# Kernel tuning notes

Hardware: AMD Instinct MI355X
Metric: run time of the kernel (lower is better)

The kernel has to match this reference:

```python
import jax, jax.numpy as jnp
import numpy as np

E = 256  # embedding_dim

def setup_inputs() -> dict:
    key = jax.random.key(0)
    k1, k2, k3 = jax.random.split(key, 3)
    B, P, N, D = 32, 4, 1024, E
    x = jax.random.normal(k1, (B, P, N, D), dtype=jnp.float32)
    W_qkv = jax.random.normal(k2, (D, 1 + 2 * E), dtype=jnp.float32) * (1.0 / np.sqrt(D))
    b_qkv = jnp.zeros((1 + 2 * E,), dtype=jnp.float32)
    W_o = jax.random.normal(k3, (E, E), dtype=jnp.float32) * (1.0 / np.sqrt(E))
    b_o = jnp.zeros((E,), dtype=jnp.float32)
    return {"x": x, "W_qkv": W_qkv, "b_qkv": b_qkv, "W_o": W_o, "b_o": b_o}

def reference(x, W_qkv, b_qkv, W_o, b_o):
    # qkv projection: [B,P,N,D] @ [D,1+2E] -> [B,P,N,1+2E]
    qkv = jnp.einsum('bpnd,de->bpne', x, W_qkv) + b_qkv
    q = qkv[..., :1]                 # [B,P,N,1]
    k = qkv[..., 1:1 + E]            # [B,P,N,E]
    v = jax.nn.relu(qkv[..., 1 + E:])  # [B,P,N,E]
    # softmax over patch axis N (axis=2)
    context_scores = jax.nn.softmax(q, axis=2)
    # context vector: sum over N of k * scores -> [B,P,1,E]
    context_vector = jnp.sum(k * context_scores, axis=2, keepdims=True)
    # broadcast-multiply with relu(v): [B,P,N,E] * [B,P,1,E]
    updated_values = v * context_vector
    # output projection
    out = jnp.einsum('bpnd,de->bpne', updated_values, W_o) + b_o
    return out
```

## Files before the change

### kernel.cpp

```cpp
#include <hip/hip_runtime.h>
#include <hip/hip_bf16.h>

typedef float f32x4 __attribute__((ext_vector_type(4)));
typedef short s16x8 __attribute__((ext_vector_type(8)));
typedef __bf16 bf16x8 __attribute__((ext_vector_type(8)));
typedef unsigned short u16;

#define NSEQ 1024
#define EDIM 256

#define WAITVM(N) asm volatile("s_waitcnt vmcnt(" #N ")" ::: "memory")

__device__ __forceinline__ u16 f2bf(float f){
  union { float f; unsigned u; } v; v.f = f;
  unsigned r = v.u + 0x7FFF + ((v.u >> 16) & 1);
  return (u16)(r >> 16);
}
__device__ __forceinline__ float bf2f(u16 b){
  union { float f; unsigned u; } v; v.u = ((unsigned)b) << 16;
  return v.f;
}

template <typename V>
__device__ __forceinline__ auto mfma_impl(V a, V b, f32x4 c, int)
    -> decltype(__builtin_amdgcn_mfma_f32_16x16x32_bf16(a, b, c, 0, 0, 0)) {
  return __builtin_amdgcn_mfma_f32_16x16x32_bf16(a, b, c, 0, 0, 0);
}
template <typename V>
__device__ __forceinline__ f32x4 mfma_impl(V a, V b, f32x4 c, long){
  bf16x8 ab = __builtin_bit_cast(bf16x8, a);
  bf16x8 bb = __builtin_bit_cast(bf16x8, b);
  return __builtin_amdgcn_mfma_f32_16x16x32_bf16(ab, bb, c, 0, 0, 0);
}
__device__ __forceinline__ f32x4 mfma16(s16x8 a, s16x8 b, f32x4 c){
  return mfma_impl(a, b, c, 0);
}

__device__ __forceinline__ void gload_lds16(const u16* g, u16* l){
  __builtin_amdgcn_global_load_lds((const __attribute__((address_space(1))) void*)g,
                                   (__attribute__((address_space(3))) void*)l, 16, 0, 0);
}

__global__ void k0_prep(const float* __restrict__ Wqkv, const float* __restrict__ Wo,
                        u16* __restrict__ wvf, u16* __restrict__ wof, float* __restrict__ wqc){
  int t = blockIdx.x * 256 + threadIdx.x;
  if (t < 16384){
    int which = t >> 13;
    int slot  = t & 8191;
    int l  = slot & 63;
    int nt = (slot >> 6) & 1;
    int ks = (slot >> 7) & 7;
    int c  = (slot >> 10) & 7;
    int row = ks*32 + 8*(l>>4);
    int col = c*32 + nt*16 + (l&15);
    s16x8 o8;
    if (which == 0){
      for (int j=0;j<8;j++) o8[j] = (short)f2bf(Wqkv[(size_t)(row+j)*513 + 257 + col]);
      *(s16x8*)(wvf + (size_t)slot*8) = o8;
    } else {
      for (int j=0;j<8;j++) o8[j] = (short)f2bf(Wo[(size_t)(row+j)*256 + col]);
      *(s16x8*)(wof + (size_t)slot*8) = o8;
    }
  } else if (t < 16384 + 256){
    int d = t - 16384;
    wqc[d] = Wqkv[(size_t)d*513];
  }
}

__global__ void k1_qfrag(const float* __restrict__ x, const float* __restrict__ wqc,
                         const float* __restrict__ bqkv, u16* __restrict__ xf, float* __restrict__ q){
  int bp = blockIdx.x >> 6, rt = blockIdx.x & 63;
  const float* xt = x + ((size_t)bp*NSEQ + rt*16) * EDIM;
  __shared__ float xl[16][260];
  int tid = threadIdx.x;
  for (int i=0;i<4;i++){
    int idx = tid + i*256;
    float4 vv = ((const float4*)xt)[idx];
    int row = idx >> 6, c4 = idx & 63;
    *(float4*)&xl[row][c4*4] = vv;
  }
  __syncthreads();
  int l = tid & 63, w = tid >> 6;
  int lo = l & 15, hi = l >> 4;
  for (int kk=0;kk<2;kk++){
    int ks = w*2 + kk;
    int k0 = ks*32 + 8*hi;
    s16x8 o8;
    for (int j=0;j<8;j++) o8[j] = (short)f2bf(xl[lo][k0+j]);
    size_t fo = ((((size_t)bp*64 + rt)*8 + ks)*64 + l) * 8;
    *(s16x8*)(xf + fo) = o8;
  }
  int c = l*4;
  float4 wv4 = *(const float4*)(wqc + c);
  float b0 = bqkv[0];
  for (int r=0;r<4;r++){
    int row = w*4 + r;
    float4 xv = *(float4*)&xl[row][c];
    float p = xv.x*wv4.x + xv.y*wv4.y + xv.z*wv4.z + xv.w*wv4.w;
    for (int o=32;o;o>>=1) p += __shfl_down(p, o);
    if (l == 0) q[(size_t)bp*NSEQ + rt*16 + row] = p + b0;
  }
}

__global__ __launch_bounds__(512) void k234(
    const u16* __restrict__ xf, const float* __restrict__ q,
    const float* __restrict__ Wqkv, const float* __restrict__ bqkv,
    float* __restrict__ cv){
  int bp = blockIdx.x;
  int tid = threadIdx.x, l = tid & 63, w = tid >> 6;
  int lo = l & 15, hi = l >> 4;
  __shared__ float sm[1024];
  __shared__ float red[16];
  __shared__ float tl[256];
  __shared__ float cvp[2][256];

  float2 v = ((const float2*)(q + (size_t)bp*NSEQ))[tid];
  float m = fmaxf(v.x, v.y);
  for (int o=32;o;o>>=1) m = fmaxf(m, __shfl_xor(m, o));
  if (l == 0) red[w] = m;
  __syncthreads();
  m = red[0];
#pragma unroll
  for (int i=1;i<8;i++) m = fmaxf(m, red[i]);
  float e0 = expf(v.x - m), e1 = expf(v.y - m);
  float ss = e0 + e1;
  for (int o=32;o;o>>=1) ss += __shfl_xor(ss, o);
  if (l == 0) red[8 + w] = ss;
  __syncthreads();
  float tot = red[8];
#pragma unroll
  for (int i=1;i<8;i++) tot += red[8 + i];
  float inv = 1.0f / tot;
  sm[2*tid]   = e0 * inv;
  sm[2*tid+1] = e1 * inv;
  __syncthreads();

  float acc[8];
#pragma unroll
  for (int j=0;j<8;j++) acc[j] = 0.f;
  const u16* base = xf + (((size_t)bp*64)*8 + w)*512 + (size_t)l*8;
  for (int rt=0; rt<64; rt++){
    s16x8 d8 = *(const s16x8*)(base + (size_t)rt*4096);
    float sv = sm[rt*16 + lo];
#pragma unroll
    for (int j=0;j<8;j++) acc[j] += sv * bf2f((u16)d8[j]);
  }
#pragma unroll
  for (int j=0;j<8;j++)
    for (int mm=1;mm<16;mm<<=1) acc[j] += __shfl_xor(acc[j], mm);
  if (lo == 0){
#pragma unroll
    for (int j=0;j<8;j++) tl[w*32 + 8*hi + j] = acc[j];
  }
  __syncthreads();

  int e = tid & 255, half = tid >> 8;
  float a = 0.f;
  for (int d = half*128; d < half*128 + 128; d++)
    a += tl[d] * Wqkv[(size_t)d*513 + 1 + e];
  cvp[half][e] = a;
  __syncthreads();
  if (tid < 256)
    cv[(size_t)bp*EDIM + tid] = bqkv[1 + tid] + cvp[0][tid] + cvp[1][tid];
}

__global__ __launch_bounds__(256, 2) void k5_main(
    const u16* __restrict__ xf, const u16* __restrict__ wvf, const u16* __restrict__ wof,
    const float* __restrict__ bqkv, const float* __restrict__ bo,
    const float* __restrict__ cv, float* __restrict__ out){
  int bp = blockIdx.x >> 3, rt = blockIdx.x & 7;
  int tid = threadIdx.x, l = tid & 63, w = tid >> 6;
  int lo = l & 15, hi = l >> 4;
  __shared__ u16 WBUF[3][16][512];
  __shared__ u16 HB[4][2][16][40];

  s16x8 af0[8], af1[8];
  {
    const u16* src0 = xf + ((((size_t)bp*64 + rt*8 + 2*w + 0)*8)*64 + l)*8;
    const u16* src1 = src0 + 4096;
#pragma unroll
    for (int ks=0;ks<8;ks++){
      af0[ks] = *(const s16x8*)(src0 + (size_t)ks*512);
      af1[ks] = *(const s16x8*)(src1 + (size_t)ks*512);
    }
  }
  const float* cvb = cv + (size_t)bp*EDIM;
  float* ob0 = out + ((size_t)bp*NSEQ + (rt*8 + 2*w + 0)*16) * EDIM;
  float* ob1 = ob0 + 16*EDIM;

  auto stage = [&](int chunk, int buf){
    const u16* base = (chunk < 8) ? (wvf + (size_t)chunk*8192) : (wof + (size_t)(chunk-8)*8192);
    const u16* gsrc = base + (size_t)(w*4)*512 + l*8;
#pragma unroll
    for (int i=0;i<4;i++) gload_lds16(gsrc + i*512, &WBUF[buf][w*4 + i][0]);
  };

  stage(0, 0);
  stage(1, 1);
  WAITVM(4);
  __builtin_amdgcn_s_barrier();
  __builtin_amdgcn_sched_barrier(0);

  s16x8 hf0[8], hf1[8];

#pragma unroll
  for (int c=0;c<16;c++){
    const int buf = c % 3;
    f32x4 acc00 = {0.f,0.f,0.f,0.f}, acc01 = acc00, acc10 = acc00, acc11 = acc00;
    auto do_mfma = [&](const s16x8 (&A0)[8], const s16x8 (&A1)[8]){
      __builtin_amdgcn_s_setprio(1);
#pragma unroll
      for (int ks=0;ks<8;ks++){
        s16x8 b0 = *(const s16x8*)&WBUF[buf][ks*2 + 0][l*8];
        s16x8 b1 = *(const s16x8*)&WBUF[buf][ks*2 + 1][l*8];
        acc00 = mfma16(A0[ks], b0, acc00);
        acc10 = mfma16(A1[ks], b0, acc10);
        acc01 = mfma16(A0[ks], b1, acc01);
        acc11 = mfma16(A1[ks], b1, acc11);
      }
      __builtin_amdgcn_s_setprio(0);
    };
    if (c < 8) do_mfma(af0, af1); else do_mfma(hf0, hf1);

    if (c < 8){
      int colA = c*32 + lo, colB = colA + 16;
      float bvA = bqkv[257 + colA], bvB = bqkv[257 + colB];
      float csA = cvb[colA],        csB = cvb[colB];
#pragma unroll
      for (int r=0;r<4;r++){
        float h00 = acc00[r] + bvA, h01 = acc01[r] + bvB;
        float h10 = acc10[r] + bvA, h11 = acc11[r] + bvB;
        HB[w][0][hi*4 + r][lo]      = f2bf(h00 > 0.f ? h00*csA : 0.f);
        HB[w][0][hi*4 + r][16 + lo] = f2bf(h01 > 0.f ? h01*csB : 0.f);
        HB[w][1][hi*4 + r][lo]      = f2bf(h10 > 0.f ? h10*csA : 0.f);
        HB[w][1][hi*4 + r][16 + lo] = f2bf(h11 > 0.f ? h11*csB : 0.f);
      }
      hf0[c] = *(const s16x8*)&HB[w][0][lo][8*hi];
      hf1[c] = *(const s16x8*)&HB[w][1][lo][8*hi];
    } else {
      int c2 = c - 8;
      int colA = c2*32 + lo, colB = colA + 16;
      float bbA = bo[colA], bbB = bo[colB];
#pragma unroll
      for (int r=0;r<4;r++){
        ob0[(size_t)(hi*4 + r)*EDIM + colA] = acc00[r] + bbA;
        ob0[(size_t)(hi*4 + r)*EDIM + colB] = acc01[r] + bbB;
        ob1[(size_t)(hi*4 + r)*EDIM + colA] = acc10[r] + bbA;
        ob1[(size_t)(hi*4 + r)*EDIM + colB] = acc11[r] + bbB;
      }
    }

    if (c + 2 <= 15) stage(c + 2, (c + 2) % 3);

    if (c < 8)       WAITVM(4);
    else if (c < 14) WAITVM(20);
    else if (c == 14) WAITVM(16);
    if (c < 15){
      __builtin_amdgcn_s_barrier();
      __builtin_amdgcn_sched_barrier(0);
    }
  }
}

extern "C" void kernel_launch(void* const* d_in, const int* in_sizes, int n_in,
                              void* d_out, int out_size, void* d_ws, size_t ws_size,
                              hipStream_t stream){
  const float* x    = (const float*)d_in[0];
  const float* Wqkv = (const float*)d_in[1];
  const float* bqkv = (const float*)d_in[2];
  const float* Wo   = (const float*)d_in[3];
  const float* bo   = (const float*)d_in[4];
  float* out = (float*)d_out;
  char* ws = (char*)d_ws;
  u16*   xf  = (u16*)(ws);
  u16*   wvf = (u16*)(ws + 67108864);
  u16*   wof = (u16*)(ws + 67239936);
  float* q   = (float*)(ws + 67371008);
  float* cvv = (float*)(ws + 69468160);
  float* wqc = (float*)(ws + 69599232);

  hipLaunchKernelGGL(k0_prep,    dim3(65),   dim3(256), 0, stream, Wqkv, Wo, wvf, wof, wqc);
  hipLaunchKernelGGL(k1_qfrag,   dim3(8192), dim3(256), 0, stream, x, wqc, bqkv, xf, q);
  hipLaunchKernelGGL(k234,       dim3(128),  dim3(512), 0, stream, xf, q, Wqkv, bqkv, cvv);
  hipLaunchKernelGGL(k5_main,    dim3(1024), dim3(256), 0, stream, xf, wvf, wof, bqkv, bo, cvv, out);
}
```

Measured before the change: 124.6 us.

## Double-buffer 64-column weight chunks and halve main-loop iterations and barriers

The main kernel's weight pipeline moves from triple-buffered 32-column chunks with lookahead of two to double-buffered 64-column chunks with lookahead of one. This halves the number of block barriers and makes each chunk do twice as many MFMAs, so each wait is amortised over more compute. The output bias is also preloaded into registers up front. In exchange, the prefetch distance is shorter, LDS use per block grows from 48KB to 64KB, and more accumulator registers are live, which could hurt occupancy at two blocks per CU.

```diff
diff --git a/kernel.cpp b/kernel.cpp
--- a/kernel.cpp
+++ b/kernel.cpp
@@ -171,8 +171,19 @@
   int bp = blockIdx.x >> 3, rt = blockIdx.x & 7;
   int tid = threadIdx.x, l = tid & 63, w = tid >> 6;
   int lo = l & 15, hi = l >> 4;
-  __shared__ u16 WBUF[3][16][512];
+  __shared__ u16 WBUF[2][16384];
   __shared__ u16 HB[4][2][16][40];
+
+  auto stage = [&](int chunk, int buf){
+    const u16* base = (chunk < 4) ? (wvf + (size_t)chunk*16384)
+                                  : (wof + (size_t)(chunk-4)*16384);
+    const u16* gsrc = base + (size_t)(w*8)*512 + l*8;
+    u16* dst = &WBUF[buf][(size_t)(w*8)*512];
+#pragma unroll
+    for (int i=0;i<8;i++) gload_lds16(gsrc + i*512, dst + i*512);
+  };
+
+  stage(0, 0);
 
   s16x8 af0[8], af1[8];
   {
@@ -185,77 +196,90 @@
     }
   }
   const float* cvb = cv + (size_t)bp*EDIM;
+  float bov[4][4];
+#pragma unroll
+  for (int cc=0;cc<4;cc++)
+#pragma unroll
+    for (int qq=0;qq<4;qq++)
+      bov[cc][qq] = bo[cc*64 + (qq>>1)*32 + (qq&1)*16 + lo];
+
   float* ob0 = out + ((size_t)bp*NSEQ + (rt*8 + 2*w + 0)*16) * EDIM;
   float* ob1 = ob0 + 16*EDIM;
 
-  auto stage = [&](int chunk, int buf){
-    const u16* base = (chunk < 8) ? (wvf + (size_t)chunk*8192) : (wof + (size_t)(chunk-8)*8192);
-    const u16* gsrc = base + (size_t)(w*4)*512 + l*8;
-#pragma unroll
-    for (int i=0;i<4;i++) gload_lds16(gsrc + i*512, &WBUF[buf][w*4 + i][0]);
-  };
-
-  stage(0, 0);
-  stage(1, 1);
-  WAITVM(4);
+  WAITVM(0);
   __builtin_amdgcn_s_barrier();
   __builtin_amdgcn_sched_barrier(0);
 
   s16x8 hf0[8], hf1[8];
 
 #pragma unroll
-  for (int c=0;c<16;c++){
-    const int buf = c % 3;
-    f32x4 acc00 = {0.f,0.f,0.f,0.f}, acc01 = acc00, acc10 = acc00, acc11 = acc00;
-    auto do_mfma = [&](const s16x8 (&A0)[8], const s16x8 (&A1)[8]){
-      __builtin_amdgcn_s_setprio(1);
-#pragma unroll
-      for (int ks=0;ks<8;ks++){
-        s16x8 b0 = *(const s16x8*)&WBUF[buf][ks*2 + 0][l*8];
-        s16x8 b1 = *(const s16x8*)&WBUF[buf][ks*2 + 1][l*8];
-        acc00 = mfma16(A0[ks], b0, acc00);
-        acc10 = mfma16(A1[ks], b0, acc10);
-        acc01 = mfma16(A0[ks], b1, acc01);
-        acc11 = mfma16(A1[ks], b1, acc11);
+  for (int c=0;c<8;c++){
+    const int buf = c & 1;
+    if (c < 7) stage(c+1, buf^1);
+
+    f32x4 acc0[4], acc1[4];
+#pragma unroll
+    for (int q=0;q<4;q++){
+      acc0[q] = f32x4{0.f,0.f,0.f,0.f};
+      acc1[q] = f32x4{0.f,0.f,0.f,0.f};
+    }
+
+    __builtin_amdgcn_s_setprio(1);
+#pragma unroll
+    for (int ks=0;ks<8;ks++){
+      s16x8 b[4];
+#pragma unroll
+      for (int q=0;q<4;q++)
+        b[q] = *(const s16x8*)&WBUF[buf][(size_t)(q>>1)*8192 + (size_t)(ks*2+(q&1))*512 + l*8];
+#pragma unroll
+      for (int q=0;q<4;q++){
+        if (c < 4){
+          acc0[q] = mfma16(af0[ks], b[q], acc0[q]);
+          acc1[q] = mfma16(af1[ks], b[q], acc1[q]);
+        } else {
+          acc0[q] = mfma16(hf0[ks], b[q], acc0[q]);
+          acc1[q] = mfma16(hf1[ks], b[q], acc1[q]);
+        }
       }
-      __builtin_amdgcn_s_setprio(0);
-    };
-    if (c < 8) do_mfma(af0, af1); else do_mfma(hf0, hf1);
-
-    if (c < 8){
-      int colA = c*32 + lo, colB = colA + 16;
-      float bvA = bqkv[257 + colA], bvB = bqkv[257 + colB];
-      float csA = cvb[colA],        csB = cvb[colB];
-#pragma unroll
-      for (int r=0;r<4;r++){
-        float h00 = acc00[r] + bvA, h01 = acc01[r] + bvB;
-        float h10 = acc10[r] + bvA, h11 = acc11[r] + bvB;
-        HB[w][0][hi*4 + r][lo]      = f2bf(h00 > 0.f ? h00*csA : 0.f);
-        HB[w][0][hi*4 + r][16 + lo] = f2bf(h01 > 0.f ? h01*csB : 0.f);
-        HB[w][1][hi*4 + r][lo]      = f2bf(h10 > 0.f ? h10*csA : 0.f);
-        HB[w][1][hi*4 + r][16 + lo] = f2bf(h11 > 0.f ? h11*csB : 0.f);
+    }
+    __builtin_amdgcn_s_setprio(0);
+
+    if (c < 4){
+#pragma unroll
+      for (int s=0;s<2;s++){
+        int colA = c*64 + s*32 + lo, colB = colA + 16;
+        float bvA = bqkv[257 + colA], bvB = bqkv[257 + colB];
+        float csA = cvb[colA],        csB = cvb[colB];
+#pragma unroll
+        for (int r=0;r<4;r++){
+          float h00 = acc0[s*2][r]   + bvA, h01 = acc0[s*2+1][r] + bvB;
+          float h10 = acc1[s*2][r]   + bvA, h11 = acc1[s*2+1][r] + bvB;
+          HB[w][0][hi*4 + r][lo]      = f2bf(h00 > 0.f ? h00*csA : 0.f);
+          HB[w][0][hi*4 + r][16 + lo] = f2bf(h01 > 0.f ? h01*csB : 0.f);
+          HB[w][1][hi*4 + r][lo]      = f2bf(h10 > 0.f ? h10*csA : 0.f);
+          HB[w][1][hi*4 + r][16 + lo] = f2bf(h11 > 0.f ? h11*csB : 0.f);
+        }
+        hf0[2*c + s] = *(const s16x8*)&HB[w][0][lo][8*hi];
+        hf1[2*c + s] = *(const s16x8*)&HB[w][1][lo][8*hi];
       }
-      hf0[c] = *(const s16x8*)&HB[w][0][lo][8*hi];
-      hf1[c] = *(const s16x8*)&HB[w][1][lo][8*hi];
     } else {
-      int c2 = c - 8;
-      int colA = c2*32 + lo, colB = colA + 16;
-      float bbA = bo[colA], bbB = bo[colB];
-#pragma unroll
-      for (int r=0;r<4;r++){
-        ob0[(size_t)(hi*4 + r)*EDIM + colA] = acc00[r] + bbA;
-        ob0[(size_t)(hi*4 + r)*EDIM + colB] = acc01[r] + bbB;
-        ob1[(size_t)(hi*4 + r)*EDIM + colA] = acc10[r] + bbA;
-        ob1[(size_t)(hi*4 + r)*EDIM + colB] = acc11[r] + bbB;
+      int c2 = c - 4;
+#pragma unroll
+      for (int s=0;s<2;s++){
+        int colA = c2*64 + s*32 + lo;
+#pragma unroll
+        for (int r=0;r<4;r++){
+          size_t ro = (size_t)(hi*4 + r)*EDIM;
+          ob0[ro + colA]      = acc0[s*2][r]   + bov[c2][s*2];
+          ob0[ro + colA + 16] = acc0[s*2+1][r] + bov[c2][s*2+1];
+          ob1[ro + colA]      = acc1[s*2][r]   + bov[c2][s*2];
+          ob1[ro + colA + 16] = acc1[s*2+1][r] + bov[c2][s*2+1];
+        }
       }
     }
 
-    if (c + 2 <= 15) stage(c + 2, (c + 2) % 3);
-
-    if (c < 8)       WAITVM(4);
-    else if (c < 14) WAITVM(20);
-    else if (c == 14) WAITVM(16);
-    if (c < 15){
+    if (c < 7){
+      if (c < 4) WAITVM(0); else WAITVM(32);
       __builtin_amdgcn_s_barrier();
       __builtin_amdgcn_sched_barrier(0);
     }
```

Result: no change. 125.1 us (+0.4%).
